# Optimization experiments

Hardware: AMD Instinct MI355X
Metric: run time of the kernel (lower is better)

The kernel has to match this reference:

```python
import jax, jax.numpy as jnp
import numpy as np

N = 100000       # nodes
E = 1600000      # edges (before self-loops)
D_IN = 128       # input feature dim
HID = 16         # hidden channels per head
HEADS = 4
D_OUT = 32       # output communities
NEG_SLOPE = 0.2  # PyG GATConv default leaky_relu slope


def setup_inputs() -> dict:
    key = jax.random.key(0)
    ks = jax.random.split(key, 10)
    s = 0.1
    x = jax.random.normal(ks[0], (N, D_IN), jnp.float32)
    edge_index = jax.random.randint(ks[1], (2, E), 0, N, dtype=jnp.int64)
    W1 = jax.random.normal(ks[2], (D_IN, HEADS * HID), jnp.float32) * s
    a_src1 = jax.random.normal(ks[3], (HEADS, HID), jnp.float32) * s
    a_dst1 = jax.random.normal(ks[4], (HEADS, HID), jnp.float32) * s
    b1 = jnp.zeros((HEADS * HID,), jnp.float32)
    W2 = jax.random.normal(ks[5], (HEADS * HID, D_OUT), jnp.float32) * s
    a_src2 = jax.random.normal(ks[6], (1, D_OUT), jnp.float32) * s
    a_dst2 = jax.random.normal(ks[7], (1, D_OUT), jnp.float32) * s
    b2 = jnp.zeros((D_OUT,), jnp.float32)
    return {"x": x, "edge_index": edge_index, "W1": W1, "a_src1": a_src1,
            "a_dst1": a_dst1, "b1": b1, "W2": W2, "a_src2": a_src2,
            "a_dst2": a_dst2, "b2": b2}


def _segment_softmax(logits, seg, n):
    # softmax over edges grouped by destination node (per head)
    m = jax.ops.segment_max(logits, seg, num_segments=n)
    m = jnp.where(jnp.isfinite(m), m, 0.0)  # guard empty segments
    e = jnp.exp(logits - m[seg])
    z = jax.ops.segment_sum(e, seg, num_segments=n)
    return e / (z[seg] + 1e-16)


def _gat_conv(x, src, dst, W, a_src, a_dst, bias, heads, out_c, concat):
    n = x.shape[0]
    h = (x @ W).reshape(n, heads, out_c)                 # [N,H,C]
    al_s = jnp.einsum('nhc,hc->nh', h, a_src)            # [N,H]
    al_d = jnp.einsum('nhc,hc->nh', h, a_dst)            # [N,H]
    logits = jax.nn.leaky_relu(al_s[src] + al_d[dst], NEG_SLOPE)  # [E,H]
    alpha = _segment_softmax(logits, dst, n)             # [E,H]
    msg = h[src] * alpha[..., None]                      # [E,H,C]
    out = jax.ops.segment_sum(msg, dst, num_segments=n)  # [N,H,C]
    out = out.reshape(n, heads * out_c) if concat else out.mean(axis=1)
    return out + bias


def reference(x, edge_index, W1, a_src1, a_dst1, b1, W2, a_src2, a_dst2, b2):
    loops = jnp.arange(N, dtype=edge_index.dtype)
    src = jnp.concatenate([edge_index[0], loops])
    dst = jnp.concatenate([edge_index[1], loops])
    h = _gat_conv(x, src, dst, W1, a_src1, a_dst1, b1, HEADS, HID, True)
    h = jax.nn.elu(h)
    return _gat_conv(h, src, dst, W2, a_src2, a_dst2, b2, 1, D_OUT, False)
```

## Files before the change

kernel.cpp:

```cpp
#include <hip/hip_runtime.h>
#include <math.h>

#define NN 100000
#define EE 1600000
#define DIN 128
#define C1 64
#define C2 32
#define NEG 0.2f

#define NB 1024
#define BSH 7
#define EPB 4096

static __device__ __forceinline__ float leaky(float x) { return x > 0.f ? x : NEG * x; }


__global__ __launch_bounds__(256) void k_chist(const int* __restrict__ ei, int* __restrict__ bhist) {
    __shared__ int h[NB];
    int t = threadIdx.x;
    for (int i = t; i < NB; i += 256) h[i] = 0;
    __syncthreads();
    int e0 = blockIdx.x * EPB;
#pragma unroll
    for (int j = 0; j < 16; j++) {
        int e = e0 + t + 256 * j;
        if (e < EE) atomicAdd(&h[ei[EE + e] >> BSH], 1);
    }
    __syncthreads();
    for (int i = t; i < NB; i += 256) {
        int c = h[i];
        if (c) atomicAdd(&bhist[i], c);
    }
}

__global__ __launch_bounds__(256) void k_bscan(const int* __restrict__ bhist,
                                               int* __restrict__ gbase, int* __restrict__ gcur) {
    __shared__ int s[256];
    int t = threadIdx.x;
    int base = t * 4;
    int v[4];
    int run = 0;
#pragma unroll
    for (int j = 0; j < 4; j++) {
        v[j] = run;
        run += bhist[base + j];
    }
    int val = run;
    s[t] = val;
    __syncthreads();
    for (int off = 1; off < 256; off <<= 1) {
        int add = (t >= off) ? s[t - off] : 0;
        __syncthreads();
        val += add;
        s[t] = val;
        __syncthreads();
    }
    int texcl = val - run;
#pragma unroll
    for (int j = 0; j < 4; j++) {
        gbase[base + j] = texcl + v[j];
        gcur[base + j] = texcl + v[j];
    }
}

__global__ __launch_bounds__(256) void k_bin(const int* __restrict__ ei, int* __restrict__ gcur,
                                             int2* __restrict__ binned) {
    __shared__ int h[NB];
    __shared__ int base[NB];
    int t = threadIdx.x;
    for (int i = t; i < NB; i += 256) h[i] = 0;
    __syncthreads();
    int e0 = blockIdx.x * EPB;
    int src[16], dst[16];
#pragma unroll
    for (int j = 0; j < 16; j++) {
        int e = e0 + t + 256 * j;
        if (e < EE) {
            src[j] = ei[e];
            dst[j] = ei[EE + e];
            atomicAdd(&h[dst[j] >> BSH], 1);
        } else
            dst[j] = -1;
    }
    __syncthreads();
    for (int i = t; i < NB; i += 256) {
        int c = h[i];
        if (c) base[i] = atomicAdd(&gcur[i], c);
        h[i] = 0;
    }
    __syncthreads();
#pragma unroll
    for (int j = 0; j < 16; j++) {
        if (dst[j] >= 0) {
            int b = dst[j] >> BSH;
            int r = atomicAdd(&h[b], 1);
            binned[base[b] + r] = make_int2(src[j], dst[j]);
        }
    }
}

__global__ __launch_bounds__(256) void k_bsort(const int2* __restrict__ binned,
                                               const int* __restrict__ gbase,
                                               const int* __restrict__ bhist,
                                               int* __restrict__ rs, int* __restrict__ deg,
                                               int* __restrict__ csr) {
    __shared__ int h[128], cur[128], sc[128];
    int b = blockIdx.x, t = threadIdx.x;
    if (t < 128) h[t] = 0;
    __syncthreads();
    int gb = gbase[b], cnt = bhist[b];
    for (int i = t; i < cnt; i += 256) atomicAdd(&h[binned[gb + i].y & 127], 1);
    __syncthreads();
    if (t < 128) sc[t] = h[t];
    __syncthreads();
    for (int off = 1; off < 128; off <<= 1) {
        int add = 0;
        if (t < 128 && t >= off) add = sc[t - off];
        __syncthreads();
        if (t < 128) sc[t] += add;
        __syncthreads();
    }
    if (t < 128) {
        int node = b * 128 + t;
        int excl = sc[t] - h[t];
        if (node < NN) {
            rs[node] = gb + excl;
            deg[node] = h[t];
        }
        cur[t] = excl;
    }
    __syncthreads();
    for (int i = t; i < cnt; i += 256) {
        int2 e = binned[gb + i];
        int r = atomicAdd(&cur[e.y & 127], 1);
        csr[gb + r] = e.x;
    }
}

__global__ __launch_bounds__(256, 2) void k_gemm1(
    const float* __restrict__ x, const float* __restrict__ W1,
    const float* __restrict__ a_s, const float* __restrict__ a_d,
    float* __restrict__ h1, float* __restrict__ als, float* __restrict__ ald) {
    __shared__ float xs[64 * 128];
    __shared__ float wsh[128 * 64];
    int t = threadIdx.x;
    int base = blockIdx.x * 64;
    for (int i = t; i < 2048; i += 256) ((float4*)wsh)[i] = ((const float4*)W1)[i];
    int maxn = NN - base;
    if (maxn > 64) maxn = 64;
    for (int i = t; i < 2048; i += 256) {
        int flat = i * 4;
        int n = flat >> 7;
        if (n < maxn) *(float4*)&xs[flat] = *(const float4*)&x[(size_t)(base + n) * 128 + (flat & 127)];
    }
    __syncthreads();
    int w = t >> 6, c = t & 63;
    int nb = w * 16;
    float acc[16];
#pragma unroll
    for (int j = 0; j < 16; j++) acc[j] = 0.f;
    for (int k = 0; k < 128; k += 4) {
        float w0 = wsh[k * 64 + c], w1 = wsh[(k + 1) * 64 + c];
        float w2 = wsh[(k + 2) * 64 + c], w3 = wsh[(k + 3) * 64 + c];
#pragma unroll
        for (int j = 0; j < 16; j++) {
            float4 xv = *(float4*)&xs[(nb + j) * 128 + k];
            acc[j] = fmaf(xv.x, w0, acc[j]);
            acc[j] = fmaf(xv.y, w1, acc[j]);
            acc[j] = fmaf(xv.z, w2, acc[j]);
            acc[j] = fmaf(xv.w, w3, acc[j]);
        }
    }
    float s_a = a_s[c], d_a = a_d[c];
    int hd = c >> 4;
#pragma unroll
    for (int j = 0; j < 16; j++) {
        int n = base + nb + j;
        float v = acc[j];
        float vs = v * s_a, vd = v * d_a;
#pragma unroll
        for (int off = 1; off < 16; off <<= 1) {
            vs += __shfl_xor(vs, off, 64);
            vd += __shfl_xor(vd, off, 64);
        }
        if (n < NN) {
            h1[(size_t)n * 64 + c] = v;
            if ((c & 15) == 0) {
                als[n * 4 + hd] = vs;
                ald[n * 4 + hd] = vd;
            }
        }
    }
}

__global__ __launch_bounds__(256) void k_edge1(
    const int* __restrict__ csr, const int* __restrict__ rs, const int* __restrict__ deg,
    const float* __restrict__ h1, const float* __restrict__ als, const float* __restrict__ ald,
    const float* __restrict__ b1, const float* __restrict__ W2,
    const float* __restrict__ as2, const float* __restrict__ ad2,
    float* __restrict__ h2, float* __restrict__ als2, float* __restrict__ ald2) {
    __shared__ float wsh[64 * 32];
    __shared__ float xld[4][64];
    __shared__ float pp[4][64][4];
    __shared__ int ss[4][64];
    int t = threadIdx.x;
    for (int i = t; i < 512; i += 256) ((float4*)wsh)[i] = ((const float4*)W2)[i];
    int w = t >> 6, lane = t & 63, hd = lane >> 4;
    int n = blockIdx.x * 4 + w;
    float4 ad4 = *(const float4*)&ald[n * 4];
    float4 an4 = *(const float4*)&als[n * 4];
    float ls0 = leaky(an4.x + ad4.x), ls1 = leaky(an4.y + ad4.y);
    float ls2 = leaky(an4.z + ad4.z), ls3 = leaky(an4.w + ad4.w);
    float z = 1.f;
    float acc = h1[n * 64 + lane];
    int s0 = rs[n], d = deg[n];
    for (int i0 = 0; i0 < d; i0 += 64) {
        int e = i0 + lane;
        int src = 0;
        float4 a4 = make_float4(-1e30f, -1e30f, -1e30f, -1e30f);
        if (e < d) {
            src = csr[s0 + e];
            a4 = *(const float4*)&als[src * 4];
        }
        float p0 = __expf(leaky(a4.x + ad4.x) - ls0);
        float p1 = __expf(leaky(a4.y + ad4.y) - ls1);
        float p2 = __expf(leaky(a4.z + ad4.z) - ls2);
        float p3 = __expf(leaky(a4.w + ad4.w) - ls3);
        ss[w][lane] = src;
        pp[w][lane][0] = p0;
        pp[w][lane][1] = p1;
        pp[w][lane][2] = p2;
        pp[w][lane][3] = p3;
        int cnt = d - i0;
        if (cnt > 64) cnt = 64;
#pragma unroll 4
        for (int i = 0; i < cnt; i++) {
            int sA = ss[w][i];
            float pA = pp[w][i][hd];
            z += pA;
            acc = fmaf(pA, h1[sA * 64 + lane], acc);
        }
    }
    float o = acc / (z + 1e-16f) + b1[lane];
    float xv = o > 0.f ? o : expm1f(o);

    xld[w][lane] = xv;
    __syncthreads();
    int hi = lane >> 5, cc = lane & 31;
    float accn = 0.f;
#pragma unroll
    for (int k = 0; k < 32; k++) {
        float xk = xld[w][hi * 32 + k];
        accn = fmaf(xk, wsh[(hi * 32 + k) * 32 + cc], accn);
    }
    accn += __shfl_xor(accn, 32, 64);
    float vs = accn * as2[cc], vd = accn * ad2[cc];
#pragma unroll
    for (int off = 1; off < 32; off <<= 1) {
        vs += __shfl_xor(vs, off, 64);
        vd += __shfl_xor(vd, off, 64);
    }
    if (lane < 32) h2[n * 32 + lane] = accn;
    if (lane == 0) {
        als2[n] = vs;
        ald2[n] = vd;
    }
}

__global__ __launch_bounds__(256) void k_edge2(
    const int* __restrict__ csr, const int* __restrict__ rs, const int* __restrict__ deg,
    const float* __restrict__ h2, const float* __restrict__ als, const float* __restrict__ ald,
    const float* __restrict__ b2, float* __restrict__ out) {
    __shared__ float2 pst[4][64];
    int t = threadIdx.x;
    int w = t >> 6, lane = t & 63;
    int n = blockIdx.x * 4 + w;
    int cc = lane & 31, half = lane >> 5;
    float ad = ald[n];
    float lself = leaky(als[n] + ad);
    float z = half == 0 ? 1.f : 0.f;
    float acc = half == 0 ? h2[n * 32 + cc] : 0.f;
    int s0 = rs[n], d = deg[n];
    for (int i0 = 0; i0 < d; i0 += 64) {
        int e = i0 + lane;
        int src = 0;
        float av = -1e30f;
        if (e < d) {
            src = csr[s0 + e];
            av = als[src];
        }
        float p = __expf(leaky(av + ad) - lself);
        pst[w][lane] = make_float2(__int_as_float(src), p);
        int cnt = d - i0;
        if (cnt > 64) cnt = 64;
#pragma unroll 4
        for (int i = half; i < cnt; i += 2) {
            float2 q = pst[w][i];
            int sA = __float_as_int(q.x);
            float pA = q.y;
            z += pA;
            acc = fmaf(pA, h2[sA * 32 + cc], acc);
        }
    }
    acc += __shfl_xor(acc, 32, 64);
    z += __shfl_xor(z, 32, 64);
    if (half == 0) out[n * 32 + cc] = acc / (z + 1e-16f) + b2[cc];
}

extern "C" void kernel_launch(void* const* d_in, const int* in_sizes, int n_in,
                              void* d_out, int out_size, void* d_ws, size_t ws_size,
                              hipStream_t stream) {
    const float* x = (const float*)d_in[0];
    const int* ei = (const int*)d_in[1];
    const float* W1 = (const float*)d_in[2];
    const float* as1 = (const float*)d_in[3];
    const float* ad1 = (const float*)d_in[4];
    const float* b1 = (const float*)d_in[5];
    const float* W2 = (const float*)d_in[6];
    const float* as2 = (const float*)d_in[7];
    const float* ad2 = (const float*)d_in[8];
    const float* b2 = (const float*)d_in[9];
    float* out = (float*)d_out;

    char* p = (char*)d_ws;
    auto alloc = [&](size_t bytes) -> char* {
        char* r = p;
        p += (bytes + 255) & ~(size_t)255;
        return r;
    };
    int* csr = (int*)alloc((size_t)EE * 4);
    int* rs = (int*)alloc((size_t)NN * 4);
    int* deg = (int*)alloc((size_t)NN * 4);
    int* bhist = (int*)alloc(NB * 4);
    int* gbase = (int*)alloc(NB * 4);
    int* gcur = (int*)alloc(NB * 4);
    float* h1 = (float*)alloc((size_t)NN * C1 * 4);
    float* als1 = (float*)alloc((size_t)NN * 4 * 4);
    float* ald1 = (float*)alloc((size_t)NN * 4 * 4);
    char* regionX = alloc((size_t)NN * C2 * 4 + (size_t)NN * 4 * 2 + 512);
    int2* binned = (int2*)regionX;
    float* h2 = (float*)regionX;
    float* als2 = (float*)(regionX + (size_t)NN * C2 * 4);
    float* ald2 = (float*)(regionX + (size_t)NN * C2 * 4 + (size_t)NN * 4);
    (void)ws_size;

    hipMemsetAsync(bhist, 0, NB * 4, stream);

    int nbin = (EE + EPB - 1) / EPB;
    k_chist<<<nbin, 256, 0, stream>>>(ei, bhist);
    k_bscan<<<1, 256, 0, stream>>>(bhist, gbase, gcur);
    k_bin<<<nbin, 256, 0, stream>>>(ei, gcur, binned);
    k_bsort<<<(NN + 127) / 128, 256, 0, stream>>>(binned, gbase, bhist, rs, deg, csr);

    k_gemm1<<<(NN + 63) / 64, 256, 0, stream>>>(x, W1, as1, ad1, h1, als1, ald1);
    k_edge1<<<NN / 4, 256, 0, stream>>>(csr, rs, deg, h1, als1, ald1, b1, W2, as2, ad2,
                                        h2, als2, ald2);
    k_edge2<<<NN / 4, 256, 0, stream>>>(csr, rs, deg, h2, als2, ald2, b2, out);
}
```

Before: 354.1 us.

## Store node features in fp16 and split edge gathers across half-waves

Stores the layer-1 and layer-2 projected node features (h1, h2) as fp16 instead of fp32, which halves the bytes moved by the random per-edge gathers in both aggregation kernels. Each lane now reads a half2 and accumulates two channels, so the edge loop is split across wave halves (layer 1) or quarters (layer 2), with shuffle reductions at the end. The cost is reduced precision in the stored features, which may affect accuracy tolerance, plus the extra reductions. The scratch region is resized to fit the binned edge array explicitly.

```diff
diff --git a/kernel.cpp b/kernel.cpp
--- a/kernel.cpp
+++ b/kernel.cpp
@@ -1,4 +1,5 @@
 #include <hip/hip_runtime.h>
+#include <hip/hip_fp16.h>
 #include <math.h>
 
 #define NN 100000
@@ -140,7 +141,7 @@
 __global__ __launch_bounds__(256, 2) void k_gemm1(
     const float* __restrict__ x, const float* __restrict__ W1,
     const float* __restrict__ a_s, const float* __restrict__ a_d,
-    float* __restrict__ h1, float* __restrict__ als, float* __restrict__ ald) {
+    __half* __restrict__ h1h, float* __restrict__ als, float* __restrict__ ald) {
     __shared__ float xs[64 * 128];
     __shared__ float wsh[128 * 64];
     int t = threadIdx.x;
@@ -184,7 +185,7 @@
             vd += __shfl_xor(vd, off, 64);
         }
         if (n < NN) {
-            h1[(size_t)n * 64 + c] = v;
+            h1h[(size_t)n * 64 + c] = __float2half(v);
             if ((c & 15) == 0) {
                 als[n * 4 + hd] = vs;
                 ald[n * 4 + hd] = vd;
@@ -195,24 +196,32 @@
 
 __global__ __launch_bounds__(256) void k_edge1(
     const int* __restrict__ csr, const int* __restrict__ rs, const int* __restrict__ deg,
-    const float* __restrict__ h1, const float* __restrict__ als, const float* __restrict__ ald,
+    const __half* __restrict__ h1h, const float* __restrict__ als, const float* __restrict__ ald,
     const float* __restrict__ b1, const float* __restrict__ W2,
     const float* __restrict__ as2, const float* __restrict__ ad2,
-    float* __restrict__ h2, float* __restrict__ als2, float* __restrict__ ald2) {
+    __half* __restrict__ h2h, float* __restrict__ als2, float* __restrict__ ald2) {
     __shared__ float wsh[64 * 32];
     __shared__ float xld[4][64];
     __shared__ float pp[4][64][4];
     __shared__ int ss[4][64];
     int t = threadIdx.x;
     for (int i = t; i < 512; i += 256) ((float4*)wsh)[i] = ((const float4*)W2)[i];
-    int w = t >> 6, lane = t & 63, hd = lane >> 4;
+    int w = t >> 6, lane = t & 63;
     int n = blockIdx.x * 4 + w;
     float4 ad4 = *(const float4*)&ald[n * 4];
     float4 an4 = *(const float4*)&als[n * 4];
     float ls0 = leaky(an4.x + ad4.x), ls1 = leaky(an4.y + ad4.y);
     float ls2 = leaky(an4.z + ad4.z), ls3 = leaky(an4.w + ad4.w);
-    float z = 1.f;
-    float acc = h1[n * 64 + lane];
+    const __half2* h1p = (const __half2*)h1h;
+    int cc = lane & 31, eh = lane >> 5;
+    int hd2 = cc >> 3;
+    float z = 0.f, acc0 = 0.f, acc1 = 0.f;
+    if (eh == 0) {
+        float2 fs = __half22float2(h1p[n * 32 + cc]);
+        z = 1.f;
+        acc0 = fs.x;
+        acc1 = fs.y;
+    }
     int s0 = rs[n], d = deg[n];
     for (int i0 = 0; i0 < d; i0 += 64) {
         int e = i0 + lane;
@@ -227,40 +236,47 @@
         float p2 = __expf(leaky(a4.z + ad4.z) - ls2);
         float p3 = __expf(leaky(a4.w + ad4.w) - ls3);
         ss[w][lane] = src;
-        pp[w][lane][0] = p0;
-        pp[w][lane][1] = p1;
-        pp[w][lane][2] = p2;
-        pp[w][lane][3] = p3;
+        *(float4*)&pp[w][lane][0] = make_float4(p0, p1, p2, p3);
         int cnt = d - i0;
         if (cnt > 64) cnt = 64;
-#pragma unroll 4
-        for (int i = 0; i < cnt; i++) {
+        for (int i = eh; i < cnt; i += 2) {
             int sA = ss[w][i];
-            float pA = pp[w][i][hd];
+            float pA = pp[w][i][hd2];
+            float2 f = __half22float2(h1p[sA * 32 + cc]);
             z += pA;
-            acc = fmaf(pA, h1[sA * 64 + lane], acc);
-        }
-    }
-    float o = acc / (z + 1e-16f) + b1[lane];
-    float xv = o > 0.f ? o : expm1f(o);
-
-    xld[w][lane] = xv;
-    __syncthreads();
-    int hi = lane >> 5, cc = lane & 31;
+            acc0 = fmaf(pA, f.x, acc0);
+            acc1 = fmaf(pA, f.y, acc1);
+        }
+    }
+    acc0 += __shfl_xor(acc0, 32, 64);
+    acc1 += __shfl_xor(acc1, 32, 64);
+    z += __shfl_xor(z, 32, 64);
+    float zi = __frcp_rn(z + 1e-16f);
+    float o0 = acc0 * zi + b1[2 * cc];
+    float o1 = acc1 * zi + b1[2 * cc + 1];
+    float xv0 = o0 > 0.f ? o0 : expm1f(o0);
+    float xv1 = o1 > 0.f ? o1 : expm1f(o1);
+    if (eh == 0) {
+        xld[w][2 * cc] = xv0;
+        xld[w][2 * cc + 1] = xv1;
+    }
+    __syncthreads();
+
+    int hi = lane >> 5, c2 = lane & 31;
     float accn = 0.f;
 #pragma unroll
     for (int k = 0; k < 32; k++) {
         float xk = xld[w][hi * 32 + k];
-        accn = fmaf(xk, wsh[(hi * 32 + k) * 32 + cc], accn);
+        accn = fmaf(xk, wsh[(hi * 32 + k) * 32 + c2], accn);
     }
     accn += __shfl_xor(accn, 32, 64);
-    float vs = accn * as2[cc], vd = accn * ad2[cc];
+    float vs = accn * as2[c2], vd = accn * ad2[c2];
 #pragma unroll
     for (int off = 1; off < 32; off <<= 1) {
         vs += __shfl_xor(vs, off, 64);
         vd += __shfl_xor(vd, off, 64);
     }
-    if (lane < 32) h2[n * 32 + lane] = accn;
+    if (lane < 32) h2h[(size_t)n * 32 + lane] = __float2half(accn);
     if (lane == 0) {
         als2[n] = vs;
         ald2[n] = vd;
@@ -269,17 +285,23 @@
 
 __global__ __launch_bounds__(256) void k_edge2(
     const int* __restrict__ csr, const int* __restrict__ rs, const int* __restrict__ deg,
-    const float* __restrict__ h2, const float* __restrict__ als, const float* __restrict__ ald,
+    const __half* __restrict__ h2h, const float* __restrict__ als, const float* __restrict__ ald,
     const float* __restrict__ b2, float* __restrict__ out) {
     __shared__ float2 pst[4][64];
     int t = threadIdx.x;
     int w = t >> 6, lane = t & 63;
     int n = blockIdx.x * 4 + w;
-    int cc = lane & 31, half = lane >> 5;
+    int cc = lane & 15, eq = lane >> 4;
     float ad = ald[n];
     float lself = leaky(als[n] + ad);
-    float z = half == 0 ? 1.f : 0.f;
-    float acc = half == 0 ? h2[n * 32 + cc] : 0.f;
+    const __half2* h2p = (const __half2*)h2h;
+    float z = 0.f, acc0 = 0.f, acc1 = 0.f;
+    if (eq == 0) {
+        float2 fs = __half22float2(h2p[n * 16 + cc]);
+        z = 1.f;
+        acc0 = fs.x;
+        acc1 = fs.y;
+    }
     int s0 = rs[n], d = deg[n];
     for (int i0 = 0; i0 < d; i0 += 64) {
         int e = i0 + lane;
@@ -293,18 +315,28 @@
         pst[w][lane] = make_float2(__int_as_float(src), p);
         int cnt = d - i0;
         if (cnt > 64) cnt = 64;
-#pragma unroll 4
-        for (int i = half; i < cnt; i += 2) {
+        for (int i = eq; i < cnt; i += 4) {
             float2 q = pst[w][i];
             int sA = __float_as_int(q.x);
             float pA = q.y;
+            float2 f = __half22float2(h2p[sA * 16 + cc]);
             z += pA;
-            acc = fmaf(pA, h2[sA * 32 + cc], acc);
-        }
-    }
-    acc += __shfl_xor(acc, 32, 64);
+            acc0 = fmaf(pA, f.x, acc0);
+            acc1 = fmaf(pA, f.y, acc1);
+        }
+    }
+    acc0 += __shfl_xor(acc0, 16, 64);
+    acc0 += __shfl_xor(acc0, 32, 64);
+    acc1 += __shfl_xor(acc1, 16, 64);
+    acc1 += __shfl_xor(acc1, 32, 64);
+    z += __shfl_xor(z, 16, 64);
     z += __shfl_xor(z, 32, 64);
-    if (half == 0) out[n * 32 + cc] = acc / (z + 1e-16f) + b2[cc];
+    if (eq == 0) {
+        float zi = __frcp_rn(z + 1e-16f);
+        float o0 = acc0 * zi + b2[2 * cc];
+        float o1 = acc1 * zi + b2[2 * cc + 1];
+        *(float2*)&out[(size_t)n * 32 + 2 * cc] = make_float2(o0, o1);
+    }
 }
 
 extern "C" void kernel_launch(void* const* d_in, const int* in_sizes, int n_in,
@@ -334,14 +366,14 @@
     int* bhist = (int*)alloc(NB * 4);
     int* gbase = (int*)alloc(NB * 4);
     int* gcur = (int*)alloc(NB * 4);
-    float* h1 = (float*)alloc((size_t)NN * C1 * 4);
+    __half* h1h = (__half*)alloc((size_t)NN * C1 * 2);
     float* als1 = (float*)alloc((size_t)NN * 4 * 4);
     float* ald1 = (float*)alloc((size_t)NN * 4 * 4);
-    char* regionX = alloc((size_t)NN * C2 * 4 + (size_t)NN * 4 * 2 + 512);
+    char* regionX = alloc((size_t)EE * 8);
     int2* binned = (int2*)regionX;
-    float* h2 = (float*)regionX;
-    float* als2 = (float*)(regionX + (size_t)NN * C2 * 4);
-    float* ald2 = (float*)(regionX + (size_t)NN * C2 * 4 + (size_t)NN * 4);
+    __half* h2h = (__half*)regionX;
+    float* als2 = (float*)(regionX + (size_t)NN * C2 * 2);
+    float* ald2 = (float*)(regionX + (size_t)NN * C2 * 2 + (size_t)NN * 4);
     (void)ws_size;
 
     hipMemsetAsync(bhist, 0, NB * 4, stream);
@@ -352,8 +384,8 @@
     k_bin<<<nbin, 256, 0, stream>>>(ei, gcur, binned);
     k_bsort<<<(NN + 127) / 128, 256, 0, stream>>>(binned, gbase, bhist, rs, deg, csr);
 
-    k_gemm1<<<(NN + 63) / 64, 256, 0, stream>>>(x, W1, as1, ad1, h1, als1, ald1);
-    k_edge1<<<NN / 4, 256, 0, stream>>>(csr, rs, deg, h1, als1, ald1, b1, W2, as2, ad2,
-                                        h2, als2, ald2);
-    k_edge2<<<NN / 4, 256, 0, stream>>>(csr, rs, deg, h2, als2, ald2, b2, out);
-}
+    k_gemm1<<<(NN + 63) / 64, 256, 0, stream>>>(x, W1, as1, ad1, h1h, als1, ald1);
+    k_edge1<<<NN / 4, 256, 0, stream>>>(csr, rs, deg, h1h, als1, ald1, b1, W2, as2, ad2,
+                                        h2h, als2, ald2);
+    k_edge2<<<NN / 4, 256, 0, stream>>>(csr, rs, deg, h2h, als2, ald2, b2, out);
+}
```

Result: slower. 369.8 us (+4.4%).
